# Optimization experiments

Hardware: AMD Instinct MI355X
Metric: run time of the kernel (lower is better)

The kernel has to match this reference:

```python
import jax, jax.numpy as jnp
import numpy as np

N = 65536      # bs * n_graphs * 32 electrodes
E = 1048576    # edges (avg degree 16)
H = 128        # first_hc (out_channels of GatedGraphConv)
IN = 5         # input node features
G = 16         # n_graphs (conv1d in-channels)
ELEC = 32
BS = 128
NC = 3


def setup_inputs() -> dict:
    key = jax.random.key(0)
    ks = jax.random.split(key, 14)
    s = 1.0 / np.sqrt(H)
    x = jax.random.normal(ks[0], (N, IN), dtype=jnp.float32)
    edge_index = jax.random.randint(ks[1], (2, E), 0, N, dtype=jnp.int32)
    edge_attr = jax.random.uniform(ks[2], (E,), dtype=jnp.float32)
    gconv_w = jax.random.normal(ks[3], (2, H, H), dtype=jnp.float32) * s
    gru_w_ih = jax.random.normal(ks[4], (3 * H, H), dtype=jnp.float32) * s
    gru_w_hh = jax.random.normal(ks[5], (3 * H, H), dtype=jnp.float32) * s
    gru_b_ih = jax.random.normal(ks[6], (3 * H,), dtype=jnp.float32) * s
    gru_b_hh = jax.random.normal(ks[7], (3 * H,), dtype=jnp.float32) * s
    conv_w = jax.random.normal(ks[8], (1, G, 3), dtype=jnp.float32) * (1.0 / np.sqrt(G * 3))
    conv_b = jax.random.normal(ks[9], (1,), dtype=jnp.float32) * 0.1
    L = (H - 3) // 2 + 1  # 63
    lin1_w = jax.random.normal(ks[10], (H, ELEC * L), dtype=jnp.float32) * (1.0 / np.sqrt(ELEC * L))
    lin1_b = jnp.zeros((H,), dtype=jnp.float32)
    lin2_w = jax.random.normal(ks[11], (NC, H), dtype=jnp.float32) * s
    lin2_b = jnp.zeros((NC,), dtype=jnp.float32)
    return {"x": x, "edge_index": edge_index, "edge_attr": edge_attr, "bs": BS,
            "gconv_w": gconv_w, "gru_w_ih": gru_w_ih, "gru_w_hh": gru_w_hh,
            "gru_b_ih": gru_b_ih, "gru_b_hh": gru_b_hh,
            "conv_w": conv_w, "conv_b": conv_b,
            "lin1_w": lin1_w, "lin1_b": lin1_b, "lin2_w": lin2_w, "lin2_b": lin2_b}


def _gated_graph_conv(x, edge_index, edge_attr, gconv_w, w_ih, w_hh, b_ih, b_hh):
    n = x.shape[0]
    # pad input features up to H (PyG GatedGraphConv behavior when in < out)
    h = jnp.concatenate([x, jnp.zeros((n, H - x.shape[1]), dtype=x.dtype)], axis=1)
    src, dst = edge_index[0], edge_index[1]
    for i in range(2):  # num_layers = 2
        m = h @ gconv_w[i]                              # [N, H]
        msg = m[src] * edge_attr[:, None]               # gather + edge weight
        agg = jax.ops.segment_sum(msg, dst, num_segments=n)  # scatter-add
        # GRUCell(agg, h)
        gi = agg @ w_ih.T + b_ih
        gh = h @ w_hh.T + b_hh
        i_r, i_z, i_n = jnp.split(gi, 3, axis=1)
        h_r, h_z, h_n = jnp.split(gh, 3, axis=1)
        r = jax.nn.sigmoid(i_r + h_r)
        z = jax.nn.sigmoid(i_z + h_z)
        nn_ = jnp.tanh(i_n + r * h_n)
        h = (1.0 - z) * nn_ + z * h
    return h


def reference(x, edge_index, edge_attr, bs, gconv_w, gru_w_ih, gru_w_hh,
              gru_b_ih, gru_b_hh, conv_w, conv_b, lin1_w, lin1_b, lin2_w, lin2_b):
    h = _gated_graph_conv(x, edge_index, edge_attr, gconv_w,
                          gru_w_ih, gru_w_hh, gru_b_ih, gru_b_hh)
    h = jax.nn.relu(h)  # dropout is identity in eval mode
    g = h.shape[0] // (bs * ELEC)
    # (bs g e) f -> (bs e) g f
    h = h.reshape(bs, g, ELEC, H).transpose(0, 2, 1, 3).reshape(bs * ELEC, g, H)
    h = jax.lax.conv_general_dilated(h, conv_w, window_strides=(2,), padding='VALID',
                                     dimension_numbers=('NCH', 'OIH', 'NCH'))
    h = h + conv_b[None, :, None]
    h = jax.nn.relu(h[:, 0, :])                 # squeeze channel -> [bs*e, L]
    h = h.reshape(bs, -1)                       # (bs e) f -> bs (e f)
    h = jax.nn.relu(h @ lin1_w.T + lin1_b)
    h = h @ lin2_w.T + lin2_b
    return jax.nn.softmax(h, axis=-1)
```

## Files before the change

kernel.cpp:

```cpp
#include <hip/hip_runtime.h>
#include <math.h>

#define NN 65536
#define NE 1048576
#define HH 128
#define ELEC 32
#define BSZ 128
#define NB 512

typedef unsigned short ushort_t;
typedef __bf16 bf16x8 __attribute__((ext_vector_type(8)));
typedef float f32x16 __attribute__((ext_vector_type(16)));

#define MFMA(A, B, C) __builtin_amdgcn_mfma_f32_32x32x16_bf16(A, B, C, 0, 0, 0)

__device__ __forceinline__ float sigm(float x) { return 1.f / (1.f + __expf(-x)); }
__device__ __forceinline__ float tanh_fast(float x) { return 2.f / (1.f + __expf(-2.f * x)) - 1.f; }

__device__ __forceinline__ float bf2f(ushort_t u) {
    union { unsigned int i; float f; } v; v.i = ((unsigned int)u) << 16; return v.f;
}
__device__ __forceinline__ ushort_t f2bf(float f) {
    union { float f; unsigned int i; } v; v.f = f;
    unsigned int r = (v.i + 0x7fffu + ((v.i >> 16) & 1u)) >> 16;
    return (ushort_t)r;
}


__global__ void k_init(const float* __restrict__ x, ushort_t* __restrict__ h) {
    int i = blockIdx.x * 256 + threadIdx.x;
    int n = i >> 7, c = i & 127;
    float v = (c < 5) ? x[n * 5 + c] : 0.f;
    h[(size_t)n * 128 + c] = f2bf(v);
}

__global__ __launch_bounds__(256) void k_bhist(const int* __restrict__ dst,
                                               int* __restrict__ bcnt) {
    __shared__ int hh[NB];
    int t = threadIdx.x;
    hh[t] = 0; hh[t + 256] = 0;
    __syncthreads();
    int e0 = blockIdx.x * 4096;
    #pragma unroll
    for (int i = 0; i < 16; ++i)
        atomicAdd(&hh[dst[e0 + i * 256 + t] >> 7], 1);
    __syncthreads();
    int c0 = hh[t];       if (c0) atomicAdd(&bcnt[t], c0);
    int c1 = hh[t + 256]; if (c1) atomicAdd(&bcnt[t + 256], c1);
}

__global__ void k_bscan(const int* __restrict__ bcnt, int* __restrict__ boffs,
                        int* __restrict__ bcur) {
    __shared__ int s[NB];
    int t = threadIdx.x;
    int v = bcnt[t];
    s[t] = v;
    __syncthreads();
    for (int d = 1; d < NB; d <<= 1) {
        int u = (t >= d) ? s[t - d] : 0;
        __syncthreads();
        s[t] += u;
        __syncthreads();
    }
    int ex = s[t] - v;
    boffs[t] = ex;
    bcur[t] = ex;
    if (t == NB - 1) boffs[NB] = s[t];
}

__global__ __launch_bounds__(256) void k_bpart(const int* __restrict__ src,
        const int* __restrict__ dst, const float* __restrict__ ea,
        int* __restrict__ bcur, uint2* __restrict__ ebkt) {
    __shared__ int lcnt[NB];
    __shared__ int base[NB];
    __shared__ int lcur[NB];
    int t = threadIdx.x;
    lcnt[t] = 0; lcnt[t + 256] = 0;
    lcur[t] = 0; lcur[t + 256] = 0;
    __syncthreads();
    int e0 = blockIdx.x * 4096;
    #pragma unroll
    for (int i = 0; i < 16; ++i)
        atomicAdd(&lcnt[dst[e0 + i * 256 + t] >> 7], 1);
    __syncthreads();
    {
        int c = lcnt[t];
        base[t] = c ? atomicAdd(&bcur[t], c) : 0;
        c = lcnt[t + 256];
        base[t + 256] = c ? atomicAdd(&bcur[t + 256], c) : 0;
    }
    __syncthreads();
    #pragma unroll
    for (int i = 0; i < 16; ++i) {
        int e = e0 + i * 256 + t;
        int d = dst[e];
        int bk = d >> 7;
        int pos = base[bk] + atomicAdd(&lcur[bk], 1);
        uint2 pk;
        pk.x = (unsigned int)src[e] | ((unsigned int)(d & 127) << 16);
        pk.y = __float_as_uint(ea[e]);
        ebkt[pos] = pk;
    }
}

__global__ __launch_bounds__(256) void k_csc(const int* __restrict__ boffs,
        const uint2* __restrict__ ebkt, uint2* __restrict__ epack,
        int* __restrict__ offs) {
    __shared__ int cnt[128];
    __shared__ int s[128];
    __shared__ int base[128];
    int b = blockIdx.x, t = threadIdx.x;
    if (t < 128) cnt[t] = 0;
    __syncthreads();
    int e0 = boffs[b], e1 = boffs[b + 1];
    for (int i = e0 + t; i < e1; i += 256)
        atomicAdd(&cnt[(ebkt[i].x >> 16) & 127], 1);
    __syncthreads();
    if (t < 128) s[t] = cnt[t];
    __syncthreads();
    for (int d = 1; d < 128; d <<= 1) {
        int v = (t < 128 && t >= d) ? s[t - d] : 0;
        __syncthreads();
        if (t < 128) s[t] += v;
        __syncthreads();
    }
    if (t < 128) {
        int bs = e0 + s[t] - cnt[t];
        base[t] = bs;
        offs[b * 128 + t] = bs;
        cnt[t] = 0;
    }
    if (b == 0 && t == 255) offs[NN] = NE;
    __syncthreads();
    for (int i = e0 + t; i < e1; i += 256) {
        uint2 e = ebkt[i];
        int dl = (e.x >> 16) & 127;
        int pos = base[dl] + atomicAdd(&cnt[dl], 1);
        epack[pos] = e;
    }
}

__global__ void k_prep(const float* __restrict__ wih, const float* __restrict__ whh,
                       const float* __restrict__ gw, const float* __restrict__ l1w,
                       ushort_t* __restrict__ vp, float* __restrict__ wt) {
    int b = blockIdx.x, t = threadIdx.x;
    if (b < 1024) {
        int i = b * 256 + t;
        int l = i >> 17, r2 = i & 131071;
        int rho = r2 >> 8, k = r2 & 255;
        int q = rho >> 7, g = (rho >> 5) & 3, cc = rho & 31;
        int c = q * 32 + cc;
        float v;
        if (k >= 128) {
            if (g == 0)      v = whh[c * 128 + k - 128];
            else if (g == 1) v = whh[(128 + c) * 128 + k - 128];
            else if (g == 2) v = 0.f;
            else             v = whh[(256 + c) * 128 + k - 128];
        } else if (g == 3) {
            v = 0.f;
        } else {
            int crow = (g == 0) ? c : ((g == 1) ? 128 + c : 256 + c);
            const float* gr = gw + l * 16384 + k * 128;
            const float* wr = wih + crow * 128;
            float s = 0.f;
            for (int j = 0; j < 128; ++j) s = fmaf(gr[j], wr[j], s);
            v = s;
        }
        int ks = k >> 4, lh = (k >> 3) & 1, j = k & 7, lr = cc;
        vp[(size_t)l * 131072 + (size_t)(ks * 16 + q * 4 + g) * 512 + (lh * 32 + lr) * 8 + j] = f2bf(v);
    } else {
        int i = (b - 1024) * 256 + t;
        int k = i >> 7, c = i & 127;
        wt[i] = l1w[c * 2016 + k];
    }
}

__global__ __launch_bounds__(256) void k_gather(const ushort_t* __restrict__ h,
        const int* __restrict__ offs, const uint2* __restrict__ epack,
        ushort_t* __restrict__ agg) {
    int n = blockIdx.x * 4 + (threadIdx.x >> 6);
    int lane = threadIdx.x & 63;
    int g = lane >> 4;
    int cj = (lane & 15) * 8;
    int k0 = offs[n], k1 = offs[n + 1];
    float a[8];
    #pragma unroll
    for (int j = 0; j < 8; ++j) a[j] = 0.f;
    int kmax = k1 - 1;
    for (int k = k0; k < k1; k += 16) {
        #pragma unroll
        for (int st = 0; st < 4; ++st) {
            int ke = k + st * 4 + g;
            uint2 e = epack[ke <= kmax ? ke : kmax];
            float w = (ke < k1) ? __uint_as_float(e.y) : 0.f;
            bf16x8 u = *reinterpret_cast<const bf16x8*>(
                h + (size_t)(e.x & 0xFFFFu) * HH + cj);
            union { bf16x8 v; ushort_t s[8]; } uu; uu.v = u;
            #pragma unroll
            for (int j = 0; j < 8; ++j)
                a[j] = fmaf(w, bf2f(uu.s[j]), a[j]);
        }
    }
    #pragma unroll
    for (int j = 0; j < 8; ++j) {
        a[j] += __shfl_xor(a[j], 16, 64);
        a[j] += __shfl_xor(a[j], 32, 64);
    }
    if (lane < 16) {
        uint4 o;
        o.x = (unsigned int)f2bf(a[0]) | ((unsigned int)f2bf(a[1]) << 16);
        o.y = (unsigned int)f2bf(a[2]) | ((unsigned int)f2bf(a[3]) << 16);
        o.z = (unsigned int)f2bf(a[4]) | ((unsigned int)f2bf(a[5]) << 16);
        o.w = (unsigned int)f2bf(a[6]) | ((unsigned int)f2bf(a[7]) << 16);
        *reinterpret_cast<uint4*>(agg + (size_t)n * 128 + cj) = o;
    }
}

__global__ __launch_bounds__(512, 4) void k_gru(const ushort_t* __restrict__ vp,
        const ushort_t* __restrict__ agg, ushort_t* __restrict__ h,
        const float* __restrict__ bih, const float* __restrict__ bhh) {
    int t = threadIdx.x;
    int lane = t & 63, w = t >> 6;
    int q = w >> 1, s = w & 1;
    int lr = lane & 31, lh = lane >> 5;
    int n0 = blockIdx.x * 64 + s * 32;
    f32x16 acc[4];
    #pragma unroll
    for (int g = 0; g < 4; ++g)
        #pragma unroll
        for (int r = 0; r < 16; ++r) acc[g][r] = 0.f;

    size_t rowA = (size_t)(n0 + lr) * 128;
    #pragma unroll
    for (int ks = 0; ks < 16; ++ks) {
        bf16x8 a;
        if (ks < 8) a = *reinterpret_cast<const bf16x8*>(agg + rowA + ks * 16 + lh * 8);
        else        a = *reinterpret_cast<const bf16x8*>(h + rowA + (ks - 8) * 16 + lh * 8);
        #pragma unroll
        for (int g = 0; g < 4; ++g) {
            bf16x8 b = *reinterpret_cast<const bf16x8*>(vp + (size_t)(ks * 16 + q * 4 + g) * 512 + lane * 8);
            acc[g] = MFMA(a, b, acc[g]);
        }
    }

    __syncthreads();

    int c = q * 32 + lr;
    float brz = bih[c] + bhh[c];
    float bzz = bih[128 + c] + bhh[128 + c];
    float bin = bih[256 + c];
    float bhn = bhh[256 + c];
    #pragma unroll
    for (int r = 0; r < 16; ++r) {
        int node = n0 + (r & 3) + 8 * (r >> 2) + 4 * lh;
        float rg = sigm(acc[0][r] + brz);
        float zg = sigm(acc[1][r] + bzz);
        float nn = tanh_fast(acc[2][r] + bin + rg * (acc[3][r] + bhn));
        size_t idx = (size_t)node * 128 + c;
        float hold = bf2f(h[idx]);
        float hnew = (1.f - zg) * nn + zg * hold;
        h[idx] = f2bf(hnew);
    }
}

__global__ __launch_bounds__(64) void k_conv(const ushort_t* __restrict__ h,
        const float* __restrict__ cw, const float* __restrict__ cb,
        float* __restrict__ co) {
    __shared__ float tile[16 * 128];
    __shared__ float w[48];
    int be = blockIdx.x;
    int b = be >> 5, e = be & 31;
    int t = threadIdx.x;
    if (t < 48) w[t] = cw[t];
    #pragma unroll
    for (int i = 0; i < 8; ++i) {
        int f = t + i * 64;
        int g = f >> 5, c4 = f & 31;
        size_t idx = (size_t)(b * 512 + g * 32 + e) * 128 + c4 * 4;
        ushort4 vh4 = *reinterpret_cast<const ushort4*>(h + idx);
        float* dst = tile + g * 128 + c4 * 4;
        dst[0] = fmaxf(bf2f(vh4.x), 0.f);
        dst[1] = fmaxf(bf2f(vh4.y), 0.f);
        dst[2] = fmaxf(bf2f(vh4.z), 0.f);
        dst[3] = fmaxf(bf2f(vh4.w), 0.f);
    }
    __syncthreads();
    if (t < 63) {
        float s = cb[0];
        #pragma unroll
        for (int g = 0; g < 16; ++g) {
            const float* p = tile + g * 128 + 2 * t;
            s = fmaf(p[0], w[g * 3 + 0], s);
            s = fmaf(p[1], w[g * 3 + 1], s);
            s = fmaf(p[2], w[g * 3 + 2], s);
        }
        co[b * 2016 + e * 63 + t] = fmaxf(s, 0.f);
    }
}

__global__ __launch_bounds__(128) void k_lin1(const float* __restrict__ co,
        const float* __restrict__ wt, float* __restrict__ fc1) {
    int b = blockIdx.x >> 3;
    int ks = blockIdx.x & 7;
    int c = threadIdx.x;
    const float* cb_ = co + b * 2016 + ks * 252;
    const float* wb = wt + (ks * 252) * 128 + c;
    float s = 0.f;
    #pragma unroll 4
    for (int k = 0; k < 252; ++k)
        s = fmaf(wb[k * 128], cb_[k], s);
    atomicAdd(&fc1[b * 128 + c], s);
}

__global__ __launch_bounds__(128) void k_lin2(const float* __restrict__ fc1,
        const float* __restrict__ l1b, const float* __restrict__ w,
        const float* __restrict__ bias, float* __restrict__ out) {
    int b = threadIdx.x;
    float s0 = bias[0], s1 = bias[1], s2 = bias[2];
    const float* v = fc1 + b * 128;
    for (int k = 0; k < 128; ++k) {
        float x = fmaxf(v[k] + l1b[k], 0.f);
        s0 = fmaf(x, w[k], s0);
        s1 = fmaf(x, w[128 + k], s1);
        s2 = fmaf(x, w[256 + k], s2);
    }
    float mx = fmaxf(s0, fmaxf(s1, s2));
    float e0 = __expf(s0 - mx), e1 = __expf(s1 - mx), e2 = __expf(s2 - mx);
    float inv = 1.f / (e0 + e1 + e2);
    out[b * 3 + 0] = e0 * inv;
    out[b * 3 + 1] = e1 * inv;
    out[b * 3 + 2] = e2 * inv;
}

extern "C" void kernel_launch(void* const* d_in, const int* in_sizes, int n_in,
                              void* d_out, int out_size, void* d_ws, size_t ws_size,
                              hipStream_t stream) {
    const float* x   = (const float*)d_in[0];
    const int*   ei  = (const int*)d_in[1];
    const float* ea  = (const float*)d_in[2];
    const float* gw  = (const float*)d_in[4];
    const float* wih = (const float*)d_in[5];
    const float* whh = (const float*)d_in[6];
    const float* bih = (const float*)d_in[7];
    const float* bhh = (const float*)d_in[8];
    const float* cw  = (const float*)d_in[9];
    const float* cb  = (const float*)d_in[10];
    const float* l1w = (const float*)d_in[11];
    const float* l1b = (const float*)d_in[12];
    const float* l2w = (const float*)d_in[13];
    const float* l2b = (const float*)d_in[14];
    float* out = (float*)d_out;

    char* p = (char*)d_ws;
    ushort_t* h   = (ushort_t*)p; p += (size_t)NN * 128 * 2;
    ushort_t* agg = (ushort_t*)p; p += (size_t)NN * 128 * 2;
    ushort_t* vp  = (ushort_t*)p; p += 2 * 512 * 256 * 2;
    uint2* ebkt   = (uint2*)p;   p += (size_t)NE * 8;
    uint2* epack  = (uint2*)p;   p += (size_t)NE * 8;
    float* wt  = (float*)p; p += 2016 * 128 * 4;
    float* co  = (float*)p; p += (size_t)BSZ * 2016 * 4;
    float* fc1 = (float*)p; p += (size_t)BSZ * HH * 4;
    int* bcnt  = (int*)p; p += NB * 4;
    int* boffs = (int*)p; p += (NB + 1) * 4;
    int* bcur  = (int*)p; p += NB * 4;
    int* offs  = (int*)p; p += (size_t)(NN + 1) * 4;

    const int* src = ei;
    const int* dst = ei + NE;

    k_prep<<<2032, 256, 0, stream>>>(wih, whh, gw, l1w, vp, wt);
    hipMemsetAsync(bcnt, 0, NB * 4, stream);
    hipMemsetAsync(fc1, 0, (size_t)BSZ * HH * 4, stream);
    k_bhist<<<256, 256, 0, stream>>>(dst, bcnt);
    k_bscan<<<1, 512, 0, stream>>>(bcnt, boffs, bcur);
    k_bpart<<<256, 256, 0, stream>>>(src, dst, ea, bcur, ebkt);
    k_csc<<<NB, 256, 0, stream>>>(boffs, ebkt, epack, offs);
    k_init<<<(NN * 128) / 256, 256, 0, stream>>>(x, h);

    for (int layer = 0; layer < 2; ++layer) {
        k_gather<<<NN / 4, 256, 0, stream>>>(h, offs, epack, agg);
        k_gru<<<NN / 64, 512, 0, stream>>>(vp + (size_t)layer * 131072, agg, h, bih, bhh);
    }

    k_conv<<<BSZ * ELEC, 64, 0, stream>>>(h, cw, cb, co);
    k_lin1<<<BSZ * 8, 128, 0, stream>>>(co, wt, fc1);
    k_lin2<<<1, 128, 0, stream>>>(fc1, l1b, l2w, l2b, out);
}
```

Baseline: 349.2 us.

## Remove memsets/atomics, fold init into prep, stage GRU weights in LDS

Folds the node-feature init kernel into k_prep and drops both memsets. The global atomic histogram and the lin1 atomic accumulation become per-block partial buffers that k_bscan and k_lin2 reduce. This cuts launches and global atomics, at the cost of a serial 256-row sum in the single-block scan. k_gru now double-buffers each weight slice through shared memory with a barrier per k-step instead of reading weights straight from global memory, which adds 32KB LDS per block and may reduce occupancy.

```diff
diff --git a/kernel.cpp b/kernel.cpp
--- a/kernel.cpp
+++ b/kernel.cpp
@@ -26,16 +26,8 @@
     return (ushort_t)r;
 }
 
-
-__global__ void k_init(const float* __restrict__ x, ushort_t* __restrict__ h) {
-    int i = blockIdx.x * 256 + threadIdx.x;
-    int n = i >> 7, c = i & 127;
-    float v = (c < 5) ? x[n * 5 + c] : 0.f;
-    h[(size_t)n * 128 + c] = f2bf(v);
-}
-
-__global__ __launch_bounds__(256) void k_bhist(const int* __restrict__ dst,
-                                               int* __restrict__ bcnt) {
+__global__ __launch_bounds__(256) void k_hist2(const int* __restrict__ dst,
+                                               int* __restrict__ bh) {
     __shared__ int hh[NB];
     int t = threadIdx.x;
     hh[t] = 0; hh[t + 256] = 0;
@@ -45,15 +37,16 @@
     for (int i = 0; i < 16; ++i)
         atomicAdd(&hh[dst[e0 + i * 256 + t] >> 7], 1);
     __syncthreads();
-    int c0 = hh[t];       if (c0) atomicAdd(&bcnt[t], c0);
-    int c1 = hh[t + 256]; if (c1) atomicAdd(&bcnt[t + 256], c1);
-}
-
-__global__ void k_bscan(const int* __restrict__ bcnt, int* __restrict__ boffs,
+    bh[blockIdx.x * NB + t] = hh[t];
+    bh[blockIdx.x * NB + t + 256] = hh[t + 256];
+}
+
+__global__ void k_bscan(const int* __restrict__ bh, int* __restrict__ boffs,
                         int* __restrict__ bcur) {
     __shared__ int s[NB];
     int t = threadIdx.x;
-    int v = bcnt[t];
+    int v = 0;
+    for (int i = 0; i < 256; ++i) v += bh[i * NB + t];
     s[t] = v;
     __syncthreads();
     for (int d = 1; d < NB; d <<= 1) {
@@ -142,7 +135,9 @@
 
 __global__ void k_prep(const float* __restrict__ wih, const float* __restrict__ whh,
                        const float* __restrict__ gw, const float* __restrict__ l1w,
-                       ushort_t* __restrict__ vp, float* __restrict__ wt) {
+                       const float* __restrict__ x,
+                       ushort_t* __restrict__ vp, float* __restrict__ wt,
+                       ushort_t* __restrict__ h) {
     int b = blockIdx.x, t = threadIdx.x;
     if (b < 1024) {
         int i = b * 256 + t;
@@ -168,10 +163,15 @@
         }
         int ks = k >> 4, lh = (k >> 3) & 1, j = k & 7, lr = cc;
         vp[(size_t)l * 131072 + (size_t)(ks * 16 + q * 4 + g) * 512 + (lh * 32 + lr) * 8 + j] = f2bf(v);
-    } else {
+    } else if (b < 2032) {
         int i = (b - 1024) * 256 + t;
         int k = i >> 7, c = i & 127;
         wt[i] = l1w[c * 2016 + k];
+    } else {
+        int i = (b - 2032) * 256 + t;
+        int n = i >> 7, c = i & 127;
+        float v = (c < 5) ? x[n * 5 + c] : 0.f;
+        h[(size_t)n * 128 + c] = f2bf(v);
     }
 }
 
@@ -219,6 +219,7 @@
 __global__ __launch_bounds__(512, 4) void k_gru(const ushort_t* __restrict__ vp,
         const ushort_t* __restrict__ agg, ushort_t* __restrict__ h,
         const float* __restrict__ bih, const float* __restrict__ bhh) {
+    __shared__ ushort_t lV[2][8192];
     int t = threadIdx.x;
     int lane = t & 63, w = t >> 6;
     int q = w >> 1, s = w & 1;
@@ -231,19 +232,41 @@
         for (int r = 0; r < 16; ++r) acc[g][r] = 0.f;
 
     size_t rowA = (size_t)(n0 + lr) * 128;
+
+    {
+        const uint4* gsrc = reinterpret_cast<const uint4*>(vp);
+        uint4 p0 = gsrc[t * 2 + 0];
+        uint4 p1 = gsrc[t * 2 + 1];
+        uint4* ld = reinterpret_cast<uint4*>(lV[0]);
+        ld[t * 2 + 0] = p0;
+        ld[t * 2 + 1] = p1;
+    }
+    __syncthreads();
+
     #pragma unroll
     for (int ks = 0; ks < 16; ++ks) {
+        uint4 p0, p1;
+        if (ks < 15) {
+            const uint4* gsrc = reinterpret_cast<const uint4*>(vp + (ks + 1) * 8192);
+            p0 = gsrc[t * 2 + 0];
+            p1 = gsrc[t * 2 + 1];
+        }
         bf16x8 a;
         if (ks < 8) a = *reinterpret_cast<const bf16x8*>(agg + rowA + ks * 16 + lh * 8);
         else        a = *reinterpret_cast<const bf16x8*>(h + rowA + (ks - 8) * 16 + lh * 8);
+        const ushort_t* lbuf = lV[ks & 1];
         #pragma unroll
-        for (int g = 0; g < 4; ++g) {
-            bf16x8 b = *reinterpret_cast<const bf16x8*>(vp + (size_t)(ks * 16 + q * 4 + g) * 512 + lane * 8);
-            acc[g] = MFMA(a, b, acc[g]);
-        }
-    }
-
-    __syncthreads();
+        for (int g2 = 0; g2 < 4; ++g2) {
+            bf16x8 b = *reinterpret_cast<const bf16x8*>(lbuf + (q * 4 + g2) * 512 + lane * 8);
+            acc[g2] = MFMA(a, b, acc[g2]);
+        }
+        if (ks < 15) {
+            uint4* ld = reinterpret_cast<uint4*>(lV[(ks + 1) & 1]);
+            ld[t * 2 + 0] = p0;
+            ld[t * 2 + 1] = p1;
+        }
+        __syncthreads();
+    }
 
     int c = q * 32 + lr;
     float brz = bih[c] + bhh[c];
@@ -299,7 +322,7 @@
 }
 
 __global__ __launch_bounds__(128) void k_lin1(const float* __restrict__ co,
-        const float* __restrict__ wt, float* __restrict__ fc1) {
+        const float* __restrict__ wt, float* __restrict__ fc1p) {
     int b = blockIdx.x >> 3;
     int ks = blockIdx.x & 7;
     int c = threadIdx.x;
@@ -309,17 +332,20 @@
     #pragma unroll 4
     for (int k = 0; k < 252; ++k)
         s = fmaf(wb[k * 128], cb_[k], s);
-    atomicAdd(&fc1[b * 128 + c], s);
-}
-
-__global__ __launch_bounds__(128) void k_lin2(const float* __restrict__ fc1,
+    fc1p[(size_t)ks * (BSZ * 128) + b * 128 + c] = s;
+}
+
+__global__ __launch_bounds__(128) void k_lin2(const float* __restrict__ fc1p,
         const float* __restrict__ l1b, const float* __restrict__ w,
         const float* __restrict__ bias, float* __restrict__ out) {
     int b = threadIdx.x;
     float s0 = bias[0], s1 = bias[1], s2 = bias[2];
-    const float* v = fc1 + b * 128;
     for (int k = 0; k < 128; ++k) {
-        float x = fmaxf(v[k] + l1b[k], 0.f);
+        float v = 0.f;
+        #pragma unroll
+        for (int ks = 0; ks < 8; ++ks)
+            v += fc1p[(size_t)ks * (BSZ * 128) + b * 128 + k];
+        float x = fmaxf(v + l1b[k], 0.f);
         s0 = fmaf(x, w[k], s0);
         s1 = fmaf(x, w[128 + k], s1);
         s2 = fmaf(x, w[256 + k], s2);
@@ -357,10 +383,10 @@
     ushort_t* vp  = (ushort_t*)p; p += 2 * 512 * 256 * 2;
     uint2* ebkt   = (uint2*)p;   p += (size_t)NE * 8;
     uint2* epack  = (uint2*)p;   p += (size_t)NE * 8;
-    float* wt  = (float*)p; p += 2016 * 128 * 4;
-    float* co  = (float*)p; p += (size_t)BSZ * 2016 * 4;
-    float* fc1 = (float*)p; p += (size_t)BSZ * HH * 4;
-    int* bcnt  = (int*)p; p += NB * 4;
+    float* wt   = (float*)p; p += 2016 * 128 * 4;
+    float* co   = (float*)p; p += (size_t)BSZ * 2016 * 4;
+    float* fc1p = (float*)p; p += 8 * (size_t)BSZ * 128 * 4;
+    int* bh    = (int*)p; p += 256 * NB * 4;
     int* boffs = (int*)p; p += (NB + 1) * 4;
     int* bcur  = (int*)p; p += NB * 4;
     int* offs  = (int*)p; p += (size_t)(NN + 1) * 4;
@@ -368,14 +394,11 @@
     const int* src = ei;
     const int* dst = ei + NE;
 
-    k_prep<<<2032, 256, 0, stream>>>(wih, whh, gw, l1w, vp, wt);
-    hipMemsetAsync(bcnt, 0, NB * 4, stream);
-    hipMemsetAsync(fc1, 0, (size_t)BSZ * HH * 4, stream);
-    k_bhist<<<256, 256, 0, stream>>>(dst, bcnt);
-    k_bscan<<<1, 512, 0, stream>>>(bcnt, boffs, bcur);
+    k_prep<<<34800, 256, 0, stream>>>(wih, whh, gw, l1w, x, vp, wt, h);
+    k_hist2<<<256, 256, 0, stream>>>(dst, bh);
+    k_bscan<<<1, 512, 0, stream>>>(bh, boffs, bcur);
     k_bpart<<<256, 256, 0, stream>>>(src, dst, ea, bcur, ebkt);
     k_csc<<<NB, 256, 0, stream>>>(boffs, ebkt, epack, offs);
-    k_init<<<(NN * 128) / 256, 256, 0, stream>>>(x, h);
 
     for (int layer = 0; layer < 2; ++layer) {
         k_gather<<<NN / 4, 256, 0, stream>>>(h, offs, epack, agg);
@@ -383,6 +406,6 @@
     }
 
     k_conv<<<BSZ * ELEC, 64, 0, stream>>>(h, cw, cb, co);
-    k_lin1<<<BSZ * 8, 128, 0, stream>>>(co, wt, fc1);
-    k_lin2<<<1, 128, 0, stream>>>(fc1, l1b, l2w, l2b, out);
-}
+    k_lin1<<<BSZ * 8, 128, 0, stream>>>(co, wt, fc1p);
+    k_lin2<<<1, 128, 0, stream>>>(fc1p, l1b, l2w, l2b, out);
+}
```

New measurement: 375.4 us. 1.08x slower.
